# Kernel optimization log

Measured on AMD Instinct MI355X. Metric: run time of the kernel, lower is better.

The kernel has to match this reference:

```python
import jax, jax.numpy as jnp
import numpy as np
from jax import lax

H = W = 96
C = 3
N_PIX = H * W
N_PER_CLASS = 50   # min(size_sample_fg=100 -> shuffled to min_samples, size_sample_bg=50)
K = 5
THRESHOLD = 0.3
POS_WEIGHT = 100.0
CLEAN_THRESH = 0.6


def _sample_idx(key, valid_mask_flat, n):
    # Uniform random sample of n indices from valid positions (fixed-shape
    # replacement for tf.random.shuffle(tf.where(mask))[:n]).
    u = jax.random.uniform(key, (N_PIX,))
    score = jnp.where(valid_mask_flat, u, -1.0)
    _, idx = lax.top_k(score, n)
    return idx


def _pixel_features(img01):
    # img01: [H, W, C] in [0, 1]. Matches: reshape(img)/255 concat weighted positions.
    img_flat = img01.reshape(-1, C) / 255.0
    ii, jj = jnp.meshgrid(jnp.arange(H), jnp.arange(W), indexing='ij')
    pos = jnp.stack([ii, jj], axis=-1).reshape(-1, 2).astype(jnp.float32)
    pos = pos / jnp.array([H, W], jnp.float32) * POS_WEIGHT
    return jnp.concatenate([img_flat, pos], axis=1)  # [N_PIX, C+2]


def _process_image(img, key):
    # preprocess: (already 96x96x3) normalize & clip
    img_p = jnp.clip(img / 255.0, 0.0, 1.0)

    # extract_image_tf: clean image, pick fg/bg scribble pixels
    img_norm = img_p / jnp.max(img_p, axis=(0, 1), keepdims=True)
    cleaned = img_norm * (img_norm < CLEAN_THRESH).astype(jnp.float32)
    fg = jnp.any(cleaned > 0, axis=-1).reshape(-1)  # [N_PIX] bool
    bg = ~fg
    k_fg, k_bg = jax.random.split(key)
    fg_idx = _sample_idx(k_fg, fg, N_PER_CLASS)
    bg_idx = _sample_idx(k_bg, bg, N_PER_CLASS)

    # extract_features_tf
    feats_all = _pixel_features(img_p)                       # [N_PIX, 5]
    train_feats = jnp.concatenate([feats_all[fg_idx], feats_all[bg_idx]], axis=0)  # [100, 5]
    train_labels = jnp.concatenate([jnp.ones(N_PER_CLASS), jnp.zeros(N_PER_CLASS)])

    # segment_image_KNN_tf: standardize, brute-force cdist, top-k, label vote
    mean = jnp.mean(train_feats, axis=0)
    std = jnp.std(train_feats, axis=0)
    train_s = (train_feats - mean) / std                     # [100, 5]
    test_s = (feats_all - mean) / std                        # [N_PIX, 5]
    dist = jnp.sqrt(jnp.sum(jnp.square(test_s[:, None, :] - train_s[None, :, :]), axis=2))  # [N_PIX, 100]
    _, knn_idx = lax.top_k(-dist, K)                         # smallest-k distances
    probas = jnp.mean(train_labels[knn_idx], axis=1)         # [N_PIX]
    seg = (probas >= THRESHOLD).astype(jnp.int32).reshape(H, W)

    # mask original (preprocessed) image
    return jnp.where(seg[..., None] == 1, img_p, jnp.zeros_like(img_p))


def setup_inputs() -> dict:
    key = jax.random.key(0)
    images = jax.random.uniform(key, (32, H, W, C), dtype=jnp.float32)
    return {"images": images}


def reference(images):
    B = images.shape[0]
    keys = jax.random.split(jax.random.key(42), B)
    return jax.vmap(_process_image)(images, keys)
```

## Files before the change

kernel.cpp:

```cpp
#include <hip/hip_runtime.h>
#include <stdint.h>

#define NPIX 9216
#define NIMG 32
#define STRIP 1152

__device__ __forceinline__ uint32_t rotl32(uint32_t x, int d){ return (x<<d)|(x>>(32-d)); }

__device__ __forceinline__ void threefry(uint32_t k0, uint32_t k1, uint32_t x0, uint32_t x1,
                                         uint32_t &o0, uint32_t &o1){
  uint32_t ks2 = k0 ^ k1 ^ 0x1BD11BDAu;
  x0 += k0; x1 += k1;
  x0+=x1; x1=rotl32(x1,13); x1^=x0;
  x0+=x1; x1=rotl32(x1,15); x1^=x0;
  x0+=x1; x1=rotl32(x1,26); x1^=x0;
  x0+=x1; x1=rotl32(x1,6);  x1^=x0;
  x0+=k1; x1+=ks2+1u;
  x0+=x1; x1=rotl32(x1,17); x1^=x0;
  x0+=x1; x1=rotl32(x1,29); x1^=x0;
  x0+=x1; x1=rotl32(x1,16); x1^=x0;
  x0+=x1; x1=rotl32(x1,24); x1^=x0;
  x0+=ks2; x1+=k0+2u;
  x0+=x1; x1=rotl32(x1,13); x1^=x0;
  x0+=x1; x1=rotl32(x1,15); x1^=x0;
  x0+=x1; x1=rotl32(x1,26); x1^=x0;
  x0+=x1; x1=rotl32(x1,6);  x1^=x0;
  x0+=k0; x1+=k1+3u;
  x0+=x1; x1=rotl32(x1,17); x1^=x0;
  x0+=x1; x1=rotl32(x1,29); x1^=x0;
  x0+=x1; x1=rotl32(x1,16); x1^=x0;
  x0+=x1; x1=rotl32(x1,24); x1^=x0;
  x0+=k1; x1+=ks2+4u;
  x0+=x1; x1=rotl32(x1,13); x1^=x0;
  x0+=x1; x1=rotl32(x1,15); x1^=x0;
  x0+=x1; x1=rotl32(x1,26); x1^=x0;
  x0+=x1; x1=rotl32(x1,6);  x1^=x0;
  x0+=ks2; x1+=k0+5u;
  o0=x0; o1=x1;
}

__device__ __forceinline__ float clip01_div255(float x){
  return fminf(fmaxf(x/255.0f, 0.0f), 1.0f);
}

__global__ __launch_bounds__(256) void kscore(const float* __restrict__ in,
                                              unsigned long long* __restrict__ key50g){
#pragma clang fp contract(off)
  int b   = blockIdx.x;
  int img = b >> 3, sub = b & 7;
  int tid = threadIdx.x;
  int lane = tid & 63, wv = tid >> 6;

  __shared__ __attribute__((aligned(16))) float pixL[3456];
  __shared__ uint32_t vvL[STRIP];
  __shared__ uint64_t cand[STRIP];
  __shared__ unsigned char fgm[STRIP];
  __shared__ int hist[129];
  __shared__ int ncand, bbin;
  __shared__ float red[3][4];

  const float* p = in + (size_t)img*NPIX*3;

  const float4* sp4 = (const float4*)(p + (size_t)sub*STRIP*3);
  float4* pixL4 = (float4*)pixL;
  for(int k=0;k<4;k++){ int i4=k*256+tid; if(i4<864) pixL4[i4]=sp4[i4]; }

  float m0=0.f,m1=0.f,m2=0.f;
  const float4* p4 = (const float4*)p;
#pragma unroll 3
  for(int k=0;k<9;k++){
    int g = tid + k*256;
    float4 v0=p4[3*g], v1=p4[3*g+1], v2=p4[3*g+2];
    m0=fmaxf(m0, fmaxf(fmaxf(clip01_div255(v0.x),clip01_div255(v0.w)),
                       fmaxf(clip01_div255(v1.z),clip01_div255(v2.y))));
    m1=fmaxf(m1, fmaxf(fmaxf(clip01_div255(v0.y),clip01_div255(v1.x)),
                       fmaxf(clip01_div255(v1.w),clip01_div255(v2.z))));
    m2=fmaxf(m2, fmaxf(fmaxf(clip01_div255(v0.z),clip01_div255(v1.y)),
                       fmaxf(clip01_div255(v2.x),clip01_div255(v2.w))));
  }
  for(int off=32;off>0;off>>=1){
    m0=fmaxf(m0,__shfl_down(m0,off));
    m1=fmaxf(m1,__shfl_down(m1,off));
    m2=fmaxf(m2,__shfl_down(m2,off));
  }
  if(lane==0){ red[0][wv]=m0; red[1][wv]=m1; red[2][wv]=m2; }
  __syncthreads();
  float c0=fmaxf(fmaxf(red[0][0],red[0][1]),fmaxf(red[0][2],red[0][3]));
  float c1=fmaxf(fmaxf(red[1][0],red[1][1]),fmaxf(red[1][2],red[1][3]));
  float c2=fmaxf(fmaxf(red[2][0],red[2][1]),fmaxf(red[2][2],red[2][3]));

  uint32_t ik0, ik1; threefry(0u, 42u, 0u, (uint32_t)img, ik0, ik1);

  for(int cls=0; cls<2; cls++){
    __syncthreads();
    if(tid<129) hist[tid]=0;
    if(tid==0)  ncand=0;
    uint32_t s0, s1; threefry(ik0, ik1, 0u, (uint32_t)cls, s0, s1);
    __syncthreads();

    for(int r=0;r<5;r++){
      int pi = tid + r*256;
      if(pi<STRIP){
        bool valid;
        if(cls==0){
          float a  = clip01_div255(pixL[pi*3+0])/c0;
          float bb = clip01_div255(pixL[pi*3+1])/c1;
          float c  = clip01_div255(pixL[pi*3+2])/c2;
          bool fg = (a>0.f && a<0.6f) || (bb>0.f && bb<0.6f) || (c>0.f && c<0.6f);
          fgm[pi] = fg ? 1 : 0;
          valid = fg;
        } else {
          valid = (fgm[pi] == 0);
        }
        uint32_t gi = (uint32_t)(sub*STRIP + pi);
        uint32_t r1,r2; threefry(s0, s1, 0u, gi, r1, r2);
        uint32_t vv = valid ? ((r1 ^ r2) >> 9) + 1u : 0u;
        vvL[pi] = vv;
        atomicAdd(&hist[vv>>16], 1);
      }
    }
    __syncthreads();

    if(tid < 64){
      int h0 = hist[2*tid];
      int h1 = hist[2*tid+1];
      int h128 = hist[128];
      int S = h0 + h1;
      for(int off=1; off<64; off<<=1){
        int o = __shfl_down(S, off);
        if(tid + off < 64) S += o;
      }
      int ss0 = S + h128;
      int ss1 = S - h0 + h128;
      int cd = -1;
      if(ss0 >= 50) cd = 2*tid;
      if(ss1 >= 50) cd = 2*tid+1;
      if(tid==63 && h128 >= 50) cd = 128;
      for(int off=32; off>0; off>>=1){
        int o = __shfl_down(cd, off);
        cd = o > cd ? o : cd;
      }
      if(tid==0) bbin = cd;
    }
    __syncthreads();

    int bb = bbin;
    for(int r=0;r<5;r++){
      int pi = tid + r*256;
      if(pi<STRIP){
        uint32_t vv = vvL[pi];
        if((int)(vv>>16) >= bb){
          int pos = atomicAdd(&ncand,1);
          cand[pos] = ((uint64_t)vv << 14) | (uint64_t)(16383 - (sub*STRIP + pi));
        }
      }
    }
    __syncthreads();
    int m = ncand;
    for(int c=tid;c<m;c+=256){
      uint64_t k = cand[c];
      int r = 0, j = 0;
      while(j < m){
        int je = j+64 < m ? j+64 : m;
        for(; j<je; j++) r += (cand[j] > k);
        if(r >= 50) break;
      }
      if(r < 50) key50g[(size_t)(img*16 + cls*8 + sub)*50 + r] = k;
    }
  }
}

__global__ __launch_bounds__(256) void kmerge(const float* __restrict__ in,
                                              const unsigned long long* __restrict__ key50g,
                                              float* __restrict__ ts2g,
                                              float* __restrict__ meanstd){
#pragma clang fp contract(off)
  int img = blockIdx.x;
  int tid = threadIdx.x;
  __shared__ uint64_t kk[800];
  __shared__ int      tIdx[100];
  __shared__ float    feat[100][5];
  __shared__ float    mv[5], sv[5];

  const uint64_t* kg = (const uint64_t*)key50g + (size_t)img*800;
  for(int c=tid;c<800;c+=256) kk[c] = kg[c];
  __syncthreads();

  for(int c=tid;c<800;c+=256){
    uint64_t k = kk[c];
    int cl = (c >= 400);
    int base = cl*400;
    int r = 0;
#pragma unroll
    for(int s=0;s<8;s++){
      const uint64_t* L = &kk[base + s*50];
      int lo=0, hi=50;
      while(lo<hi){ int mid=(lo+hi)>>1; if(L[mid] > k) lo=mid+1; else hi=mid; }
      r += lo;
    }
    if(r < 50) tIdx[cl*50+r] = 16383 - (int)(k & 16383u);
  }
  __syncthreads();

  if(tid<100){
    int pp = tIdx[tid];
    int i=pp/96, j=pp-i*96;
    const float* px = in + ((size_t)img*NPIX + pp)*3;
    for(int c=0;c<3;c++){
      float ip=clip01_div255(px[c]);
      feat[tid][c]=ip/255.0f;
    }
    feat[tid][3]=((float)i/96.0f)*100.0f;
    feat[tid][4]=((float)j/96.0f)*100.0f;
  }
  __syncthreads();
  if(tid<5){
    float s=0.f;
    for(int r=0;r<100;r++) s=s+feat[r][tid];
    float mu=s/100.0f; mv[tid]=mu;
    float v=0.f;
    for(int r=0;r<100;r++){ float d=feat[r][tid]-mu; float q=d*d; v=v+q; }
    sv[tid]=sqrtf(v/100.0f);
  }
  __syncthreads();
  if(tid<100){
    float r0=(feat[tid][0]-mv[0])/sv[0];
    float r1=(feat[tid][1]-mv[1])/sv[1];
    float r2=(feat[tid][2]-mv[2])/sv[2];
    float r3=(feat[tid][3]-mv[3])/sv[3];
    float r4=(feat[tid][4]-mv[4])/sv[4];
    float* dst = ts2g + img*600 + (tid>>1)*12 + (tid&1);
    dst[0]=r0; dst[2]=r1; dst[4]=r2; dst[6]=r3; dst[8]=r4;
  }
  if(tid<5)       meanstd[img*10+tid]=mv[tid];
  else if(tid<10) meanstd[img*10+tid]=sv[tid-5];
}

__global__ __launch_bounds__(256) void kknn(const float* __restrict__ in,
                                            const float* __restrict__ ts2g,
                                            const float* __restrict__ meanstd,
                                            float* __restrict__ out){
#pragma clang fp contract(off)
  int b     = blockIdx.x;
  int img   = b / 36;
  int chunk = b % 36;
  int tid   = threadIdx.x;

  __shared__ float    mv[5], sv[5];
  __shared__ __attribute__((aligned(16))) float ts2[600];
  __shared__ __attribute__((aligned(16))) float pix[768];

  if(tid<150) ((float4*)ts2)[tid] = ((const float4*)(ts2g + img*600))[tid];
  if(tid>=192 && tid<197) mv[tid-192]=meanstd[img*10+(tid-192)];
  if(tid>=224 && tid<229) sv[tid-224]=meanstd[img*10+5+(tid-224)];
  {
    const float4* cb4 = (const float4*)(in + ((size_t)img*NPIX + (size_t)chunk*256)*3);
    if(tid<192) ((float4*)pix)[tid] = cb4[tid];
  }
  __syncthreads();

  int p = chunk*256+tid;
  int i=p/96, j=p-i*96;
  float ip0=clip01_div255(pix[tid*3+0]);
  float ip1=clip01_div255(pix[tid*3+1]);
  float ip2=clip01_div255(pix[tid*3+2]);
  float t0,t1,t2,t3,t4;
  {
    float f0=ip0/255.0f, f1=ip1/255.0f, f2=ip2/255.0f;
    float f3=((float)i/96.0f)*100.0f, f4=((float)j/96.0f)*100.0f;
    t0=(f0-mv[0])/sv[0]; t1=(f1-mv[1])/sv[1]; t2=(f2-mv[2])/sv[2];
    t3=(f3-mv[3])/sv[3]; t4=(f4-mv[4])/sv[4];
  }

  float a0x=1e30f,a0y=1e30f, a1x=1e30f,a1y=1e30f;
#pragma unroll 5
  for(int pr=0;pr<25;pr++){
    const float* tp = &ts2[pr*12];
    float4 qA = *(const float4*)(tp);
    float4 qB = *(const float4*)(tp+4);
    float2 qC = *(const float2*)(tp+8);
    float sx, sy;
    { float dx=t0-qA.x, dy=t0-qA.y; sx=dx*dx; sy=dy*dy; }
    { float dx=t1-qA.z, dy=t1-qA.w; float wx=dx*dx, wy=dy*dy; sx=sx+wx; sy=sy+wy; }
    { float dx=t2-qB.x, dy=t2-qB.y; float wx=dx*dx, wy=dy*dy; sx=sx+wx; sy=sy+wy; }
    { float dx=t3-qB.z, dy=t3-qB.w; float wx=dx*dx, wy=dy*dy; sx=sx+wx; sy=sy+wy; }
    { float dx=t4-qC.x, dy=t4-qC.y; float wx=dx*dx, wy=dy*dy; sx=sx+wx; sy=sy+wy; }
    float tx=fmaxf(a0x,sx), ty=fmaxf(a0y,sy);
    a0x=fminf(a0x,sx);      a0y=fminf(a0y,sy);
    a1x=fminf(a1x,tx);      a1y=fminf(a1y,ty);
  }
  float a1 = fmaxf(fminf(a0x,a1y), fminf(a1x,a0y));

  float b0x=1e30f,b0y=1e30f, b1x=1e30f,b1y=1e30f;
  float b2x=1e30f,b2y=1e30f, b3x=1e30f,b3y=1e30f;
#pragma unroll 5
  for(int pr=25;pr<50;pr++){
    const float* tp = &ts2[pr*12];
    float4 qA = *(const float4*)(tp);
    float4 qB = *(const float4*)(tp+4);
    float2 qC = *(const float2*)(tp+8);
    float sx, sy;
    { float dx=t0-qA.x, dy=t0-qA.y; sx=dx*dx; sy=dy*dy; }
    { float dx=t1-qA.z, dy=t1-qA.w; float wx=dx*dx, wy=dy*dy; sx=sx+wx; sy=sy+wy; }
    { float dx=t2-qB.x, dy=t2-qB.y; float wx=dx*dx, wy=dy*dy; sx=sx+wx; sy=sy+wy; }
    { float dx=t3-qB.z, dy=t3-qB.w; float wx=dx*dx, wy=dy*dy; sx=sx+wx; sy=sy+wy; }
    { float dx=t4-qC.x, dy=t4-qC.y; float wx=dx*dx, wy=dy*dy; sx=sx+wx; sy=sy+wy; }
    float u0x=fmaxf(b0x,sx), u0y=fmaxf(b0y,sy);
    b0x=fminf(b0x,sx);       b0y=fminf(b0y,sy);
    float u1x=fmaxf(b1x,u0x), u1y=fmaxf(b1y,u0y);
    b1x=fminf(b1x,u0x);       b1y=fminf(b1y,u0y);
    float u2x=fmaxf(b2x,u1x), u2y=fmaxf(b2y,u1y);
    b2x=fminf(b2x,u1x);       b2y=fminf(b2y,u1y);
    b3x=fminf(b3x,u2x);       b3y=fminf(b3y,u2y);
  }
  float l0=fminf(b0x,b3y), l1=fminf(b1x,b2y), l2=fminf(b2x,b1y), l3=fminf(b3x,b0y);
  float b3 = fmaxf(fmaxf(l0,l1), fmaxf(l2,l3));

  bool seg = sqrtf(a1) <= sqrtf(b3);
  __syncthreads();
  pix[tid*3+0]=seg?ip0:0.f;
  pix[tid*3+1]=seg?ip1:0.f;
  pix[tid*3+2]=seg?ip2:0.f;
  __syncthreads();
  float4* ob4 = (float4*)(out + ((size_t)img*NPIX + (size_t)chunk*256)*3);
  if(tid<192) ob4[tid] = ((float4*)pix)[tid];
}

extern "C" void kernel_launch(void* const* d_in, const int* in_sizes, int n_in,
                              void* d_out, int out_size, void* d_ws, size_t ws_size,
                              hipStream_t stream) {
  const float* in = (const float*)d_in[0];
  float* out = (float*)d_out;
  unsigned long long* key50g = (unsigned long long*)d_ws;
  float* ts2g    = (float*)((char*)d_ws + 204800);
  float* meanstd = (float*)((char*)d_ws + 281600);

  kscore<<<256,  256, 0, stream>>>(in, key50g);
  kmerge<<<32,   256, 0, stream>>>(in, key50g, ts2g, meanstd);
  kknn  <<<1152, 256, 0, stream>>>(in, ts2g, meanstd, out);
}
```

Before: 110.0 us.

## Split per-image max into separate kernel and parallelize kscore over class

Moves the per-image channel max reduction out of kscore into a new kmax kernel of 192 blocks that writes partial maxima. Each of the 256 kscore blocks previously re-read the whole image to compute that max. kscore now launches 512 blocks, one per image, class and strip, so the fg and bg sampling run in parallel instead of in a sequential loop. The cost is an extra kernel launch, the fg mask being recomputed per class, and the strip being loaded twice.

Result: faster. 103.7 us (-5.7%).

```diff
diff --git a/kernel.cpp b/kernel.cpp
--- a/kernel.cpp
+++ b/kernel.cpp
@@ -43,21 +43,54 @@
   return fminf(fmaxf(x/255.0f, 0.0f), 1.0f);
 }
 
+__global__ __launch_bounds__(256) void kmax(const float* __restrict__ in,
+                                            float* __restrict__ maxpart){
+  int img  = blockIdx.x / 6;
+  int part = blockIdx.x % 6;
+  int tid  = threadIdx.x;
+  const float* base = in + (size_t)img*NPIX*3 + (size_t)part*1536*3;
+  float m0=0.f, m1=0.f, m2=0.f;
+#pragma unroll
+  for(int k=0;k<18;k++){
+    int g = k*256 + tid;
+    float v = clip01_div255(base[g]);
+    int c = g % 3;
+    m0 = (c==0) ? fmaxf(m0,v) : m0;
+    m1 = (c==1) ? fmaxf(m1,v) : m1;
+    m2 = (c==2) ? fmaxf(m2,v) : m2;
+  }
+  for(int off=32; off>0; off>>=1){
+    m0 = fmaxf(m0, __shfl_down(m0,off));
+    m1 = fmaxf(m1, __shfl_down(m1,off));
+    m2 = fmaxf(m2, __shfl_down(m2,off));
+  }
+  __shared__ float r[3][4];
+  int lane = tid & 63, wv = tid >> 6;
+  if(lane==0){ r[0][wv]=m0; r[1][wv]=m1; r[2][wv]=m2; }
+  __syncthreads();
+  if(tid==0){
+    maxpart[blockIdx.x*3+0]=fmaxf(fmaxf(r[0][0],r[0][1]),fmaxf(r[0][2],r[0][3]));
+    maxpart[blockIdx.x*3+1]=fmaxf(fmaxf(r[1][0],r[1][1]),fmaxf(r[1][2],r[1][3]));
+    maxpart[blockIdx.x*3+2]=fmaxf(fmaxf(r[2][0],r[2][1]),fmaxf(r[2][2],r[2][3]));
+  }
+}
+
 __global__ __launch_bounds__(256) void kscore(const float* __restrict__ in,
+                                              const float* __restrict__ maxpart,
                                               unsigned long long* __restrict__ key50g){
 #pragma clang fp contract(off)
   int b   = blockIdx.x;
-  int img = b >> 3, sub = b & 7;
+  int img = b >> 4, cls = (b >> 3) & 1, sub = b & 7;
   int tid = threadIdx.x;
-  int lane = tid & 63, wv = tid >> 6;
 
   __shared__ __attribute__((aligned(16))) float pixL[3456];
   __shared__ uint32_t vvL[STRIP];
   __shared__ uint64_t cand[STRIP];
-  __shared__ unsigned char fgm[STRIP];
   __shared__ int hist[129];
   __shared__ int ncand, bbin;
-  __shared__ float red[3][4];
+
+  if(tid<129) hist[tid]=0;
+  if(tid==0)  ncand=0;
 
   const float* p = in + (size_t)img*NPIX*3;
 
@@ -65,108 +98,80 @@
   float4* pixL4 = (float4*)pixL;
   for(int k=0;k<4;k++){ int i4=k*256+tid; if(i4<864) pixL4[i4]=sp4[i4]; }
 
-  float m0=0.f,m1=0.f,m2=0.f;
-  const float4* p4 = (const float4*)p;
-#pragma unroll 3
-  for(int k=0;k<9;k++){
-    int g = tid + k*256;
-    float4 v0=p4[3*g], v1=p4[3*g+1], v2=p4[3*g+2];
-    m0=fmaxf(m0, fmaxf(fmaxf(clip01_div255(v0.x),clip01_div255(v0.w)),
-                       fmaxf(clip01_div255(v1.z),clip01_div255(v2.y))));
-    m1=fmaxf(m1, fmaxf(fmaxf(clip01_div255(v0.y),clip01_div255(v1.x)),
-                       fmaxf(clip01_div255(v1.w),clip01_div255(v2.z))));
-    m2=fmaxf(m2, fmaxf(fmaxf(clip01_div255(v0.z),clip01_div255(v1.y)),
-                       fmaxf(clip01_div255(v2.x),clip01_div255(v2.w))));
-  }
-  for(int off=32;off>0;off>>=1){
-    m0=fmaxf(m0,__shfl_down(m0,off));
-    m1=fmaxf(m1,__shfl_down(m1,off));
-    m2=fmaxf(m2,__shfl_down(m2,off));
-  }
-  if(lane==0){ red[0][wv]=m0; red[1][wv]=m1; red[2][wv]=m2; }
-  __syncthreads();
-  float c0=fmaxf(fmaxf(red[0][0],red[0][1]),fmaxf(red[0][2],red[0][3]));
-  float c1=fmaxf(fmaxf(red[1][0],red[1][1]),fmaxf(red[1][2],red[1][3]));
-  float c2=fmaxf(fmaxf(red[2][0],red[2][1]),fmaxf(red[2][2],red[2][3]));
+  float c0=0.f,c1=0.f,c2=0.f;
+#pragma unroll
+  for(int s=0;s<6;s++){
+    c0=fmaxf(c0, maxpart[(img*6+s)*3+0]);
+    c1=fmaxf(c1, maxpart[(img*6+s)*3+1]);
+    c2=fmaxf(c2, maxpart[(img*6+s)*3+2]);
+  }
 
   uint32_t ik0, ik1; threefry(0u, 42u, 0u, (uint32_t)img, ik0, ik1);
-
-  for(int cls=0; cls<2; cls++){
-    __syncthreads();
-    if(tid<129) hist[tid]=0;
-    if(tid==0)  ncand=0;
-    uint32_t s0, s1; threefry(ik0, ik1, 0u, (uint32_t)cls, s0, s1);
-    __syncthreads();
-
-    for(int r=0;r<5;r++){
-      int pi = tid + r*256;
-      if(pi<STRIP){
-        bool valid;
-        if(cls==0){
-          float a  = clip01_div255(pixL[pi*3+0])/c0;
-          float bb = clip01_div255(pixL[pi*3+1])/c1;
-          float c  = clip01_div255(pixL[pi*3+2])/c2;
-          bool fg = (a>0.f && a<0.6f) || (bb>0.f && bb<0.6f) || (c>0.f && c<0.6f);
-          fgm[pi] = fg ? 1 : 0;
-          valid = fg;
-        } else {
-          valid = (fgm[pi] == 0);
-        }
-        uint32_t gi = (uint32_t)(sub*STRIP + pi);
-        uint32_t r1,r2; threefry(s0, s1, 0u, gi, r1, r2);
-        uint32_t vv = valid ? ((r1 ^ r2) >> 9) + 1u : 0u;
-        vvL[pi] = vv;
-        atomicAdd(&hist[vv>>16], 1);
+  uint32_t s0, s1;   threefry(ik0, ik1, 0u, (uint32_t)cls, s0, s1);
+  __syncthreads();
+
+  for(int r=0;r<5;r++){
+    int pi = tid + r*256;
+    if(pi<STRIP){
+      float a  = clip01_div255(pixL[pi*3+0])/c0;
+      float bb = clip01_div255(pixL[pi*3+1])/c1;
+      float c  = clip01_div255(pixL[pi*3+2])/c2;
+      bool fg = (a>0.f && a<0.6f) || (bb>0.f && bb<0.6f) || (c>0.f && c<0.6f);
+      bool valid = (cls==0) ? fg : !fg;
+      uint32_t gi = (uint32_t)(sub*STRIP + pi);
+      uint32_t r1,r2; threefry(s0, s1, 0u, gi, r1, r2);
+      uint32_t vv = valid ? ((r1 ^ r2) >> 9) + 1u : 0u;
+      vvL[pi] = vv;
+      if(vv) atomicAdd(&hist[vv>>16], 1);
+    }
+  }
+  __syncthreads();
+
+  if(tid < 64){
+    int h0 = hist[2*tid];
+    int h1 = hist[2*tid+1];
+    int h128 = hist[128];
+    int S = h0 + h1;
+    for(int off=1; off<64; off<<=1){
+      int o = __shfl_down(S, off);
+      if(tid + off < 64) S += o;
+    }
+    int ss0 = S + h128;
+    int ss1 = S - h0 + h128;
+    int cd = -1;
+    if(ss0 >= 50) cd = 2*tid;
+    if(ss1 >= 50) cd = 2*tid+1;
+    if(tid==63 && h128 >= 50) cd = 128;
+    for(int off=32; off>0; off>>=1){
+      int o = __shfl_down(cd, off);
+      cd = o > cd ? o : cd;
+    }
+    if(tid==0) bbin = cd;
+  }
+  __syncthreads();
+
+  int bb = bbin;
+  for(int r=0;r<5;r++){
+    int pi = tid + r*256;
+    if(pi<STRIP){
+      uint32_t vv = vvL[pi];
+      if((int)(vv>>16) >= bb){
+        int pos = atomicAdd(&ncand,1);
+        cand[pos] = ((uint64_t)vv << 14) | (uint64_t)(16383 - (sub*STRIP + pi));
       }
     }
-    __syncthreads();
-
-    if(tid < 64){
-      int h0 = hist[2*tid];
-      int h1 = hist[2*tid+1];
-      int h128 = hist[128];
-      int S = h0 + h1;
-      for(int off=1; off<64; off<<=1){
-        int o = __shfl_down(S, off);
-        if(tid + off < 64) S += o;
-      }
-      int ss0 = S + h128;
-      int ss1 = S - h0 + h128;
-      int cd = -1;
-      if(ss0 >= 50) cd = 2*tid;
-      if(ss1 >= 50) cd = 2*tid+1;
-      if(tid==63 && h128 >= 50) cd = 128;
-      for(int off=32; off>0; off>>=1){
-        int o = __shfl_down(cd, off);
-        cd = o > cd ? o : cd;
-      }
-      if(tid==0) bbin = cd;
-    }
-    __syncthreads();
-
-    int bb = bbin;
-    for(int r=0;r<5;r++){
-      int pi = tid + r*256;
-      if(pi<STRIP){
-        uint32_t vv = vvL[pi];
-        if((int)(vv>>16) >= bb){
-          int pos = atomicAdd(&ncand,1);
-          cand[pos] = ((uint64_t)vv << 14) | (uint64_t)(16383 - (sub*STRIP + pi));
-        }
-      }
-    }
-    __syncthreads();
-    int m = ncand;
-    for(int c=tid;c<m;c+=256){
-      uint64_t k = cand[c];
-      int r = 0, j = 0;
-      while(j < m){
-        int je = j+64 < m ? j+64 : m;
-        for(; j<je; j++) r += (cand[j] > k);
-        if(r >= 50) break;
-      }
-      if(r < 50) key50g[(size_t)(img*16 + cls*8 + sub)*50 + r] = k;
-    }
+  }
+  __syncthreads();
+  int m = ncand;
+  for(int c=tid;c<m;c+=256){
+    uint64_t k = cand[c];
+    int r = 0, j = 0;
+    while(j < m){
+      int je = j+64 < m ? j+64 : m;
+      for(; j<je; j++) r += (cand[j] > k);
+      if(r >= 50) break;
+    }
+    if(r < 50) key50g[(size_t)b*50 + r] = k;
   }
 }
 
@@ -331,11 +336,13 @@
                               hipStream_t stream) {
   const float* in = (const float*)d_in[0];
   float* out = (float*)d_out;
-  unsigned long long* key50g = (unsigned long long*)d_ws;
-  float* ts2g    = (float*)((char*)d_ws + 204800);
-  float* meanstd = (float*)((char*)d_ws + 281600);
-
-  kscore<<<256,  256, 0, stream>>>(in, key50g);
+  float* maxpart = (float*)d_ws;
+  unsigned long long* key50g = (unsigned long long*)((char*)d_ws + 2304);
+  float* ts2g    = (float*)((char*)d_ws + 207104);
+  float* meanstd = (float*)((char*)d_ws + 283904);
+
+  kmax  <<<192,  256, 0, stream>>>(in, maxpart);
+  kscore<<<512,  256, 0, stream>>>(in, maxpart, key50g);
   kmerge<<<32,   256, 0, stream>>>(in, key50g, ts2g, meanstd);
   kknn  <<<1152, 256, 0, stream>>>(in, ts2g, meanstd, out);
 }
```
